# Kernel optimization log

Hardware: AMD Instinct MI355X
Metric: run time of the kernel (lower is better)

## Reference

```python
import jax, jax.numpy as jnp
import numpy as np


def _sparse_mask(T, S, W, G):
    """Replicates CustomSparseAttention._create_sparse_mask (bool [T, S])."""
    ii = np.arange(T)[:, None]
    jj = np.arange(S)[None, :]
    # local sliding window: cols in [i - W//2, i + W//2]
    m = (jj >= ii - W // 2) & (jj <= ii + W // 2)
    # overlapping block windows every (W - W//4) rows
    ov = W // 4
    for i in range(0, T, W - ov):
        m[i:i + W, max(0, i - ov):min(S, i + W + ov)] = True
    # strided global tokens
    if G > 0:
        stride = S // (G + 1)
        gi = np.linspace(stride, S - stride, G).astype(np.int64)  # torch .long() truncates
        m[:, gi] = True
    # diagonal +/- 1
    m |= np.abs(jj - ii) <= 1
    return jnp.asarray(m)


def setup_inputs() -> dict:
    key = jax.random.key(0)
    ks = jax.random.split(key, 8)
    B, T, S, E = 2, 2048, 2048, 512
    std = 0.02
    return {
        "query": jax.random.normal(ks[0], (B, T, E), jnp.float32),
        "key": jax.random.normal(ks[1], (B, S, E), jnp.float32),
        "value": jax.random.normal(ks[2], (B, S, E), jnp.float32),
        "Wq": jax.random.normal(ks[3], (E, E), jnp.float32) * std,
        "bq": jnp.zeros((E,), jnp.float32),
        "Wk": jax.random.normal(ks[4], (E, E), jnp.float32) * std,
        "bk": jnp.zeros((E,), jnp.float32),
        "Wv": jax.random.normal(ks[5], (E, E), jnp.float32) * std,
        "bv": jnp.zeros((E,), jnp.float32),
        "Wo": jax.random.normal(ks[6], (E, E), jnp.float32) * std,
        "bo": jnp.zeros((E,), jnp.float32),
        "temperature": jnp.ones((1,), jnp.float32) * 0.1,
        "local_window_size": 128,
        "num_global_tokens": 16,
    }


def reference(query, key, value, Wq, bq, Wk, bk, Wv, bv, Wo, bo,
              temperature, local_window_size, num_global_tokens):
    B, T, E = query.shape
    S = key.shape[1]
    H = 16
    hd = E // H
    scaling = float(hd) ** -0.5

    q = (query @ Wq.T + bq) * scaling          # [B, T, E]
    k = key @ Wk.T + bk                        # [B, S, E]
    v = value @ Wv.T + bv                      # [B, S, E]

    q = q.reshape(B, T, H, hd)
    k = k.reshape(B, S, H, hd)
    v = v.reshape(B, S, H, hd)

    # [B, H, T, S] dense scores, scaled by learned temperature
    attn = jnp.einsum('bthd,bshd->bhts', q, k) * temperature[0]

    mask = _sparse_mask(T, S, local_window_size, num_global_tokens)  # [T, S] bool
    attn = jnp.where(mask[None, None], attn, -jnp.inf)

    # (row-max subtraction in the original is the standard stable softmax)
    attn = jax.nn.softmax(attn, axis=-1)

    out = jnp.einsum('bhts,bshd->bthd', attn, v).reshape(B, T, E)
    out = out @ Wo.T + bo
    return out
```

## Files before the change

### kernel.cpp

```cpp
#include <hip/hip_runtime.h>

typedef _Float16 f16x8 __attribute__((ext_vector_type(8)));
typedef float f32x4 __attribute__((ext_vector_type(4)));

#define Tt 2048
#define Ee 512
#define Hh 16
#define HD 32
#define Bb 2
#define Mm (Bb*Tt)

__device__ __constant__ int GCOLS[16] = {120,240,361,481,602,722,843,963,
                                         1084,1204,1325,1445,1566,1686,1807,1928};

__device__ __forceinline__ int lo_of(int i) {
    int kmin = (i >= 32) ? ((i - 32) / 96) : 0;
    int lo = kmin * 96 - 32;
    return lo < 0 ? 0 : lo;
}
__device__ __forceinline__ int hi_of(int i) {
    int hi = (i / 96) * 96 + 160;
    return hi > Tt ? Tt : hi;
}

__device__ __forceinline__ f16x8 cvt8(float4 a, float4 b) {
    f16x8 r;
    r[0]=(_Float16)a.x; r[1]=(_Float16)a.y; r[2]=(_Float16)a.z; r[3]=(_Float16)a.w;
    r[4]=(_Float16)b.x; r[5]=(_Float16)b.y; r[6]=(_Float16)b.z; r[7]=(_Float16)b.w;
    return r;
}

__device__ __forceinline__ void async_copy16(const _Float16* g, _Float16* l) {
    __builtin_amdgcn_global_load_lds(
        (const __attribute__((address_space(1))) void*)g,
        (__attribute__((address_space(3))) void*)l, 16, 0, 0);
}

__global__ __launch_bounds__(256)
void proj_kernel(const float* __restrict__ qx, const float* __restrict__ kx,
                 const float* __restrict__ vx,
                 const float* __restrict__ Wq, const float* __restrict__ Wk,
                 const float* __restrict__ Wv, const float* __restrict__ Wo,
                 const float* __restrict__ bq, const float* __restrict__ bk,
                 const float* __restrict__ bv, const float* __restrict__ temp,
                 _Float16* __restrict__ q_ws, _Float16* __restrict__ k_ws,
                 _Float16* __restrict__ v_ws, _Float16* __restrict__ wof)
{
    const int z = blockIdx.z;
    const float* A = (z == 0) ? qx : (z == 1) ? kx : vx;
    const float* W = (z == 0) ? Wq : (z == 1) ? Wk : Wv;
    const float* bias = (z == 0) ? bq : (z == 1) ? bk : bv;

    {
        const int fb = blockIdx.x + 64 * blockIdx.y + 256 * blockIdx.z;
        if (fb < 128) {
            const int g8 = fb * 256 + threadIdx.x;
            const float* src = Wo + (size_t)g8 * 8;
            float4 a = ((const float4*)src)[0];
            float4 b = ((const float4*)src)[1];
            *(f16x8*)(wof + (size_t)g8 * 8) = cvt8(a, b);
        }
    }

    const int m0 = blockIdx.x * 64;
    const int n0 = blockIdx.y * 128;

    __shared__ _Float16 Ash[64 * 64];
    __shared__ _Float16 Bsh[128 * 64];

    const int tid  = threadIdx.x;
    const int lane = tid & 63, wave = tid >> 6;
    const int quad = lane >> 4, l16 = lane & 15;
    const int wm = wave & 1, wn = wave >> 1;

    const int sl = lane >> 3;
    const int lcol = ((lane & 7) ^ sl) * 8;
    const float* aS[2] = {
        A + (size_t)(m0 + wave*8      + sl) * Ee + lcol,
        A + (size_t)(m0 + (4+wave)*8  + sl) * Ee + lcol };
    const float* bS[4] = {
        W + (size_t)(n0 + wave*8      + sl) * Ee + lcol,
        W + (size_t)(n0 + (4+wave)*8  + sl) * Ee + lcol,
        W + (size_t)(n0 + (8+wave)*8  + sl) * Ee + lcol,
        W + (size_t)(n0 + (12+wave)*8 + sl) * Ee + lcol };
    _Float16* aD[2] = { Ash + wave*512 + lane*8, Ash + (4+wave)*512 + lane*8 };
    _Float16* bD[4] = { Bsh + wave*512 + lane*8, Bsh + (4+wave)*512 + lane*8,
                        Bsh + (8+wave)*512 + lane*8, Bsh + (12+wave)*512 + lane*8 };

    float4 pa[2][2][2];
    float4 pb[2][4][2];

    #pragma unroll
    for (int u = 0; u < 2; ++u) {
        pa[0][u][0] = ((const float4*)(aS[u]))[0];
        pa[0][u][1] = ((const float4*)(aS[u]))[1];
    }
    #pragma unroll
    for (int u = 0; u < 4; ++u) {
        pb[0][u][0] = ((const float4*)(bS[u]))[0];
        pb[0][u][1] = ((const float4*)(bS[u]))[1];
    }

    f32x4 acc[2][4] = {};

    #pragma unroll
    for (int it = 0; it < 8; ++it) {
        const int cur = it & 1, nxt = cur ^ 1;

        __syncthreads();
        #pragma unroll
        for (int u = 0; u < 2; ++u)
            *(f16x8*)aD[u] = cvt8(pa[cur][u][0], pa[cur][u][1]);
        #pragma unroll
        for (int u = 0; u < 4; ++u)
            *(f16x8*)bD[u] = cvt8(pb[cur][u][0], pb[cur][u][1]);

        if (it < 7) {
            const int k0 = (it + 1) * 64;
            #pragma unroll
            for (int u = 0; u < 2; ++u) {
                pa[nxt][u][0] = ((const float4*)(aS[u] + k0))[0];
                pa[nxt][u][1] = ((const float4*)(aS[u] + k0))[1];
            }
            #pragma unroll
            for (int u = 0; u < 4; ++u) {
                pb[nxt][u][0] = ((const float4*)(bS[u] + k0))[0];
                pb[nxt][u][1] = ((const float4*)(bS[u] + k0))[1];
            }
        }
        __syncthreads();

        #pragma unroll
        for (int kk = 0; kk < 2; kk++) {
            f16x8 af[2], bf[4];
            #pragma unroll
            for (int mt = 0; mt < 2; mt++) {
                const int row = wm*32 + mt*16 + l16;
                af[mt] = *(const f16x8*)&Ash[row*64 + (((kk*4+quad) ^ (row & 7)) * 8)];
            }
            #pragma unroll
            for (int nt = 0; nt < 4; nt++) {
                const int row = wn*64 + nt*16 + l16;
                bf[nt] = *(const f16x8*)&Bsh[row*64 + (((kk*4+quad) ^ (row & 7)) * 8)];
            }
            #pragma unroll
            for (int mt = 0; mt < 2; mt++)
                #pragma unroll
                for (int nt = 0; nt < 4; nt++)
                    acc[mt][nt] = __builtin_amdgcn_mfma_f32_16x16x32_f16(af[mt], bf[nt], acc[mt][nt], 0, 0, 0);
        }
    }

    const float scale = (z == 0) ? (0.17677669529663687f * temp[0]) : 1.0f;
    #pragma unroll
    for (int nt = 0; nt < 4; nt++) {
        const int n = n0 + wn * 64 + nt * 16 + l16;
        const float bn = bias[n];
        const int h = n >> 5, d = n & 31;
        #pragma unroll
        for (int mt = 0; mt < 2; mt++) {
            #pragma unroll
            for (int r = 0; r < 4; r++) {
                const int m = m0 + wm * 32 + mt * 16 + quad * 4 + r;
                const float val = (acc[mt][nt][r] + bn) * scale;
                const int bidx = m >> 11, t = m & (Tt - 1);
                if (z == 2) {
                    v_ws[((size_t)(bidx * Hh + h) * HD + d) * Tt + t] = (_Float16)val;
                } else {
                    _Float16* dst = (z == 0) ? q_ws : k_ws;
                    dst[((size_t)(bidx * Hh + h) * Tt + t) * HD + d] = (_Float16)val;
                }
            }
        }
    }
}

__global__ __launch_bounds__(256)
void attn_kernel(const _Float16* __restrict__ q_ws, const _Float16* __restrict__ k_ws,
                 const _Float16* __restrict__ v_ws, _Float16* __restrict__ o_ws)
{
    const int qb = blockIdx.x * 64;
    const int h  = blockIdx.y;
    const int b  = blockIdx.z;
    const int bh = b * Hh + h;

    const int tid  = threadIdx.x;
    const int lane = tid & 63, wave = tid >> 6;
    const int quad = lane >> 4, l16 = lane & 15;
    const int t0   = qb + wave * 16;

    __shared__ _Float16 P_lds[4][16*72];
    _Float16* myP = &P_lds[wave][0];

    const f16x8 qf = *(const f16x8*)(q_ws + ((size_t)bh*Tt + t0 + l16)*HD + quad*8);

    int lo[4], len[4];
    #pragma unroll
    for (int r = 0; r < 4; r++) {
        const int i = t0 + quad*4 + r;
        lo[r] = lo_of(i); len[r] = hi_of(i) - lo[r];
    }

    float lsum[4] = {0.f, 0.f, 0.f, 0.f};
    f32x4 accO[2] = {};
    const f32x4 zf = {0.f, 0.f, 0.f, 0.f};

    {
        const int gj = GCOLS[l16];
        const f16x8 kg = *(const f16x8*)(k_ws + ((size_t)bh*Tt + gj)*HD + quad*8);
        const f32x4 s = __builtin_amdgcn_mfma_f32_16x16x32_f16(qf, kg, zf, 0, 0, 0);
        #pragma unroll
        for (int r = 0; r < 4; r++) {
            const bool inside = (unsigned)(gj - lo[r]) < (unsigned)len[r];
            const float p = inside ? 0.f : __expf(s[r]);
            const _Float16 ph = (_Float16)p;
            lsum[r] += (float)ph;
            myP[(quad*4 + r)*72 + l16] = ph;
        }
        f16x8 pf;
        if (quad < 2) pf = *(const f16x8*)&myP[l16*72 + quad*8];
        else {
            #pragma unroll
            for (int j = 0; j < 8; j++) pf[j] = (_Float16)0.f;
        }
        int gck[8];
        #pragma unroll
        for (int j = 0; j < 8; j++) gck[j] = (quad < 2) ? GCOLS[quad*8 + j] : 0;
        #pragma unroll
        for (int dt = 0; dt < 2; dt++) {
            f16x8 vg;
            if (quad < 2) {
                const _Float16* vrow = v_ws + ((size_t)bh*HD + dt*16 + l16)*Tt;
                #pragma unroll
                for (int j = 0; j < 8; j++) vg[j] = vrow[gck[j]];
            } else {
                #pragma unroll
                for (int j = 0; j < 8; j++) vg[j] = (_Float16)0.f;
            }
            accO[dt] = __builtin_amdgcn_mfma_f32_16x16x32_f16(pf, vg, accO[dt], 0, 0, 0);
        }
    }

    const int cstart = lo_of(t0) & ~63;
    const int cend   = hi_of(t0 + 15);
    for (int j0 = cstart; j0 < cend; j0 += 64) {
        f16x8 kf[4]; f32x4 s[4];
        #pragma unroll
        for (int nt = 0; nt < 4; nt++)
            kf[nt] = *(const f16x8*)(k_ws + ((size_t)bh*Tt + j0 + nt*16 + l16)*HD + quad*8);
        #pragma unroll
        for (int nt = 0; nt < 4; nt++)
            s[nt] = __builtin_amdgcn_mfma_f32_16x16x32_f16(qf, kf[nt], zf, 0, 0, 0);
        #pragma unroll
        for (int nt = 0; nt < 4; nt++) {
            const int j = j0 + nt*16 + l16;
            #pragma unroll
            for (int r = 0; r < 4; r++) {
                const bool inside = (unsigned)(j - lo[r]) < (unsigned)len[r];
                const float p = inside ? __expf(s[nt][r]) : 0.f;
                const _Float16 ph = (_Float16)p;
                lsum[r] += (float)ph;
                myP[(quad*4 + r)*72 + nt*16 + l16] = ph;
            }
        }
        #pragma unroll
        for (int kt = 0; kt < 2; kt++) {
            const f16x8 pf = *(const f16x8*)&myP[l16*72 + kt*32 + quad*8];
            #pragma unroll
            for (int dt = 0; dt < 2; dt++) {
                const f16x8 vf = *(const f16x8*)(v_ws + ((size_t)bh*HD + dt*16 + l16)*Tt
                                                 + j0 + kt*32 + quad*8);
                accO[dt] = __builtin_amdgcn_mfma_f32_16x16x32_f16(pf, vf, accO[dt], 0, 0, 0);
            }
        }
    }

    #pragma unroll
    for (int r = 0; r < 4; r++) {
        float v = lsum[r];
        v += __shfl_xor(v, 1);
        v += __shfl_xor(v, 2);
        v += __shfl_xor(v, 4);
        v += __shfl_xor(v, 8);
        lsum[r] = 1.0f / v;
    }
    #pragma unroll
    for (int dt = 0; dt < 2; dt++) {
        #pragma unroll
        for (int r = 0; r < 4; r++) {
            const int t = t0 + quad*4 + r;
            const int d = dt*16 + l16;
            o_ws[((size_t)(b*Tt + t)*Hh + h)*HD + d] = (_Float16)(accO[dt][r] * lsum[r]);
        }
    }
}

__global__ __launch_bounds__(256)
void out_kernel(const _Float16* __restrict__ Aw, const _Float16* __restrict__ Wof,
                const float* __restrict__ bo, float* __restrict__ out)
{
    const int m0 = blockIdx.x * 64;
    const int n0 = blockIdx.y * 128;

    __shared__ _Float16 Ash[64 * 64];
    __shared__ _Float16 Bsh[128 * 64];

    const int tid  = threadIdx.x;
    const int lane = tid & 63, wave = tid >> 6;
    const int quad = lane >> 4, l16 = lane & 15;
    const int wm = wave & 1, wn = wave >> 1;

    const int sl = lane >> 3;
    const int lcol = ((lane & 7) ^ sl) * 8;
    const _Float16* aSrc0 = Aw  + (size_t)(m0 + wave*8      + sl) * Ee + lcol;
    const _Float16* aSrc1 = Aw  + (size_t)(m0 + (4+wave)*8  + sl) * Ee + lcol;
    const _Float16* bSrc0 = Wof + (size_t)(n0 + wave*8      + sl) * Ee + lcol;
    const _Float16* bSrc1 = Wof + (size_t)(n0 + (4+wave)*8  + sl) * Ee + lcol;
    const _Float16* bSrc2 = Wof + (size_t)(n0 + (8+wave)*8  + sl) * Ee + lcol;
    const _Float16* bSrc3 = Wof + (size_t)(n0 + (12+wave)*8 + sl) * Ee + lcol;

    f32x4 acc[2][4] = {};

    for (int k0 = 0; k0 < Ee; k0 += 64) {
        __syncthreads();
        async_copy16(aSrc0 + k0, Ash + wave*512);
        async_copy16(aSrc1 + k0, Ash + (4+wave)*512);
        async_copy16(bSrc0 + k0, Bsh + wave*512);
        async_copy16(bSrc1 + k0, Bsh + (4+wave)*512);
        async_copy16(bSrc2 + k0, Bsh + (8+wave)*512);
        async_copy16(bSrc3 + k0, Bsh + (12+wave)*512);
        __syncthreads();

        #pragma unroll
        for (int kk = 0; kk < 2; kk++) {
            f16x8 af[2], bf[4];
            #pragma unroll
            for (int mt = 0; mt < 2; mt++) {
                const int row = wm*32 + mt*16 + l16;
                af[mt] = *(const f16x8*)&Ash[row*64 + (((kk*4+quad) ^ (row & 7)) * 8)];
            }
            #pragma unroll
            for (int nt = 0; nt < 4; nt++) {
                const int row = wn*64 + nt*16 + l16;
                bf[nt] = *(const f16x8*)&Bsh[row*64 + (((kk*4+quad) ^ (row & 7)) * 8)];
            }
            #pragma unroll
            for (int mt = 0; mt < 2; mt++)
                #pragma unroll
                for (int nt = 0; nt < 4; nt++)
                    acc[mt][nt] = __builtin_amdgcn_mfma_f32_16x16x32_f16(af[mt], bf[nt], acc[mt][nt], 0, 0, 0);
        }
    }

    #pragma unroll
    for (int nt = 0; nt < 4; nt++) {
        const int n = n0 + wn * 64 + nt * 16 + l16;
        const float bn = bo[n];
        #pragma unroll
        for (int mt = 0; mt < 2; mt++) {
            #pragma unroll
            for (int r = 0; r < 4; r++) {
                const int m = m0 + wm * 32 + mt * 16 + quad * 4 + r;
                out[(size_t)m * Ee + n] = acc[mt][nt][r] + bn;
            }
        }
    }
}

extern "C" void kernel_launch(void* const* d_in, const int* in_sizes, int n_in,
                              void* d_out, int out_size, void* d_ws, size_t ws_size,
                              hipStream_t stream)
{
    const float* query = (const float*)d_in[0];
    const float* key_  = (const float*)d_in[1];
    const float* value = (const float*)d_in[2];
    const float* Wq    = (const float*)d_in[3];
    const float* bq    = (const float*)d_in[4];
    const float* Wk    = (const float*)d_in[5];
    const float* bk    = (const float*)d_in[6];
    const float* Wv    = (const float*)d_in[7];
    const float* bv    = (const float*)d_in[8];
    const float* Wo    = (const float*)d_in[9];
    const float* bo    = (const float*)d_in[10];
    const float* temp  = (const float*)d_in[11];

    _Float16* xw   = (_Float16*)d_ws;
    _Float16* q_ws = xw + 7340032;
    _Float16* k_ws = q_ws + (size_t)Mm * Ee;
    _Float16* v_ws = k_ws + (size_t)Mm * Ee;
    _Float16* o_ws = v_ws + (size_t)Mm * Ee;
    _Float16* wof  = xw + (size_t)3 * Mm * Ee + (size_t)3 * Ee * Ee;
    float* out = (float*)d_out;

    proj_kernel<<<dim3(64, 4, 3), 256, 0, stream>>>(query, key_, value,
                                                    Wq, Wk, Wv, Wo,
                                                    bq, bk, bv, temp,
                                                    q_ws, k_ws, v_ws, wof);
    attn_kernel<<<dim3(32, 16, 2), 256, 0, stream>>>(q_ws, k_ws, v_ws, o_ws);
    out_kernel<<<dim3(64, 4), 256, 0, stream>>>(o_ws, wof, bo, out);
}
```

Measured before the change: 144.3 us.

## Split attention key range across wave pairs and reduce partial results via LDS

Each 16-row query tile is now handled by two waves. Each wave takes alternating 64-column key chunks, and one of them also processes the global tokens. The partial output accumulators and row sums are merged through shared memory after a block barrier, and the grid is doubled. This adds parallelism to the short per-wave loop so more waves are in flight across the GPU. The cost is duplicated Q loads, an LDS reduction and a __syncthreads.

Result: no change. 145.0 us (+0.5%).

```diff
diff --git a/kernel.cpp b/kernel.cpp
--- a/kernel.cpp
+++ b/kernel.cpp
@@ -179,7 +179,6 @@
 void attn_kernel(const _Float16* __restrict__ q_ws, const _Float16* __restrict__ k_ws,
                  const _Float16* __restrict__ v_ws, _Float16* __restrict__ o_ws)
 {
-    const int qb = blockIdx.x * 64;
     const int h  = blockIdx.y;
     const int b  = blockIdx.z;
     const int bh = b * Hh + h;
@@ -187,9 +186,12 @@
     const int tid  = threadIdx.x;
     const int lane = tid & 63, wave = tid >> 6;
     const int quad = lane >> 4, l16 = lane & 15;
-    const int t0   = qb + wave * 16;
+    const int pair = wave >> 1;
+    const int wsub = wave & 1;
+    const int t0   = blockIdx.x * 32 + pair * 16;
 
     __shared__ _Float16 P_lds[4][16*72];
+    __shared__ float    red[2][12][64];
     _Float16* myP = &P_lds[wave][0];
 
     const f16x8 qf = *(const f16x8*)(q_ws + ((size_t)bh*Tt + t0 + l16)*HD + quad*8);
@@ -205,7 +207,7 @@
     f32x4 accO[2] = {};
     const f32x4 zf = {0.f, 0.f, 0.f, 0.f};
 
-    {
+    if (wsub == 1) {
         const int gj = GCOLS[l16];
         const f16x8 kg = *(const f16x8*)(k_ws + ((size_t)bh*Tt + gj)*HD + quad*8);
         const f32x4 s = __builtin_amdgcn_mfma_f32_16x16x32_f16(qf, kg, zf, 0, 0, 0);
@@ -243,7 +245,7 @@
 
     const int cstart = lo_of(t0) & ~63;
     const int cend   = hi_of(t0 + 15);
-    for (int j0 = cstart; j0 < cend; j0 += 64) {
+    for (int j0 = cstart + wsub*64; j0 < cend; j0 += 128) {
         f16x8 kf[4]; f32x4 s[4];
         #pragma unroll
         for (int nt = 0; nt < 4; nt++)
@@ -275,22 +277,44 @@
         }
     }
 
-    #pragma unroll
-    for (int r = 0; r < 4; r++) {
-        float v = lsum[r];
-        v += __shfl_xor(v, 1);
-        v += __shfl_xor(v, 2);
-        v += __shfl_xor(v, 4);
-        v += __shfl_xor(v, 8);
-        lsum[r] = 1.0f / v;
-    }
-    #pragma unroll
-    for (int dt = 0; dt < 2; dt++) {
+    if (wsub == 1) {
+        #pragma unroll
+        for (int dt = 0; dt < 2; dt++)
+            #pragma unroll
+            for (int r = 0; r < 4; r++)
+                red[pair][dt*4 + r][lane] = accO[dt][r];
+        #pragma unroll
+        for (int r = 0; r < 4; r++)
+            red[pair][8 + r][lane] = lsum[r];
+    }
+    __syncthreads();
+    if (wsub == 0) {
+        #pragma unroll
+        for (int dt = 0; dt < 2; dt++)
+            #pragma unroll
+            for (int r = 0; r < 4; r++)
+                accO[dt][r] += red[pair][dt*4 + r][lane];
+        #pragma unroll
+        for (int r = 0; r < 4; r++)
+            lsum[r] += red[pair][8 + r][lane];
+
         #pragma unroll
         for (int r = 0; r < 4; r++) {
-            const int t = t0 + quad*4 + r;
-            const int d = dt*16 + l16;
-            o_ws[((size_t)(b*Tt + t)*Hh + h)*HD + d] = (_Float16)(accO[dt][r] * lsum[r]);
+            float v = lsum[r];
+            v += __shfl_xor(v, 1);
+            v += __shfl_xor(v, 2);
+            v += __shfl_xor(v, 4);
+            v += __shfl_xor(v, 8);
+            lsum[r] = 1.0f / v;
+        }
+        #pragma unroll
+        for (int dt = 0; dt < 2; dt++) {
+            #pragma unroll
+            for (int r = 0; r < 4; r++) {
+                const int t = t0 + quad*4 + r;
+                const int d = dt*16 + l16;
+                o_ws[((size_t)(b*Tt + t)*Hh + h)*HD + d] = (_Float16)(accO[dt][r] * lsum[r]);
+            }
         }
     }
 }
@@ -396,6 +420,6 @@
                                                     Wq, Wk, Wv, Wo,
                                                     bq, bk, bv, temp,
                                                     q_ws, k_ws, v_ws, wof);
-    attn_kernel<<<dim3(32, 16, 2), 256, 0, stream>>>(q_ws, k_ws, v_ws, o_ws);
+    attn_kernel<<<dim3(64, 16, 2), 256, 0, stream>>>(q_ws, k_ws, v_ws, o_ws);
     out_kernel<<<dim3(64, 4), 256, 0, stream>>>(o_ws, wof, bo, out);
 }
```
